# Optimization experiments

Hardware: AMD Instinct MI355X
Metric: run time of the kernel (lower is better)

## Reference

```python
import jax, jax.numpy as jnp
import numpy as np

DN = ('NCDHW', 'OIDHW', 'NCDHW')

def conv3(x, w):
    # 3x3x3 VALID stencil conv: [1,1,D+2,H+2,W+2] -> [1,1,D,H,W]
    return jax.lax.conv_general_dilated(x, w, (1, 1, 1), 'VALID', dimension_numbers=DN)

def conv_res(x, w):
    # 2x2x2 stride-2 restriction
    return jax.lax.conv_general_dilated(x, w, (2, 2, 2), 'VALID', dimension_numbers=DN)

def prol(x):
    for ax in (2, 3, 4):
        x = jnp.repeat(x, 2, axis=ax)
    return x

def with_halo(x, factor=1.0):
    # apply_BC_* + halo_exchange on one device: edge-replicate a 1-cell halo,
    # optionally scaled by `factor` (apply_BC_u uses -1.0 -> no-slip wall).
    p = jnp.pad(x, ((0, 0), (0, 0), (1, 1), (1, 1), (1, 1)), mode='edge')
    if factor != 1.0:
        interior = jnp.pad(jnp.ones_like(x), ((0, 0), (0, 0), (1, 1), (1, 1), (1, 1)))
        p = p * (interior + factor * (1.0 - interior))
    return p

def pad0(x):
    # apply_BC_cw: zero halo for the multigrid correction
    return jnp.pad(x, ((0, 0), (0, 0), (1, 1), (1, 1), (1, 1)))


def setup_inputs() -> dict:
    key = jax.random.key(0)
    ks = jax.random.split(key, 12)
    D = 128
    shp = (1, 1, D, D, D)
    f32 = jnp.float32
    values_u = jax.random.normal(ks[0], shp, f32)
    values_v = jax.random.normal(ks[1], shp, f32)
    values_w = jax.random.normal(ks[2], shp, f32)
    values_p = jax.random.normal(ks[3], shp, f32)
    sigma = jax.random.uniform(ks[4], shp, f32)
    kshape = (1, 1, 3, 3, 3)
    w_xadv = 0.1 * jax.random.normal(ks[5], kshape, f32)
    w_yadv = 0.1 * jax.random.normal(ks[6], kshape, f32)
    w_zadv = 0.1 * jax.random.normal(ks[7], kshape, f32)
    w_diff = 0.1 * jax.random.normal(ks[8], kshape, f32)
    wA = 0.1 * jax.random.normal(ks[9], kshape, f32)
    wA = wA.at[0, 0, 1, 1, 1].add(-6.0)  # Laplacian-like diagonal so Jacobi division is stable
    w_res = 0.1 * jax.random.normal(ks[10], (1, 1, 2, 2, 2), f32)
    dt = 0.05 * jnp.ones((1,), f32)
    return dict(values_u=values_u, values_v=values_v, values_w=values_w,
                values_p=values_p, sigma=sigma, w_xadv=w_xadv, w_yadv=w_yadv,
                w_zadv=w_zadv, w_diff=w_diff, wA=wA, w_res=w_res, dt=dt,
                iteration=2, nlevel=9)


def reference(values_u, values_v, values_w, values_p, sigma, w_xadv, w_yadv,
              w_zadv, w_diff, wA, w_res, dt, iteration, nlevel):
    diag = wA[0, 0, 1, 1, 1]
    xadv = lambda t: conv3(t, w_xadv)
    yadv = lambda t: conv3(t, w_yadv)
    zadv = lambda t: conv3(t, w_zadv)
    diff = lambda t: conv3(t, w_diff)
    A = lambda t: conv3(t, wA)

    def solid(a, b, c):
        d = 1.0 + dt * sigma
        return a / d, b / d, c / d

    def PG(uu, vv, ww, u, v, w):
        # k_u/k_v/k_w are ones; k_uu/k_vv/k_ww are their BC+halo versions (also ones)
        k_h = with_halo(jnp.ones_like(u))
        k_u = 0.5 * (diff(uu) + diff(uu * k_h) - u * diff(k_h))
        k_v = 0.5 * (diff(vv) + diff(vv * k_h) - v * diff(k_h))
        k_w = 0.5 * (diff(ww) + diff(ww * k_h) - w * diff(k_h))
        return k_u, k_v, k_w

    def f_cycle_mg(uu, vv, wwh, p, pp):
        b = -(xadv(uu) + yadv(vv) + zadv(wwh)) / dt
        w_mg = jnp.zeros((1, 1, 1, 1, 1), p.dtype)
        r = b
        for _ in range(iteration):
            w_mg = jnp.zeros((1, 1, 1, 1, 1), p.dtype)
            r = A(pp) - b
            r_s = [r]
            for _i in range(1, nlevel - 1):
                r = conv_res(r, w_res)
                r_s.append(r)
            for i in reversed(range(1, nlevel - 1)):
                ww_ = pad0(w_mg)
                w_mg = w_mg - A(ww_) / diag + r_s[i] / diag
                w_mg = prol(w_mg)
            p = p - w_mg
            p = p - A(pp) / diag + b / diag
            pp = with_halo(p)
        return p, w_mg, r, pp

    u, v, w = solid(values_u, values_v, values_w)
    uu = with_halo(u, -1.0)
    vv = with_halo(v)
    wwh = with_halo(w)
    pp = with_halo(values_p)

    k_u, k_v, k_w = PG(uu, vv, wwh, u, v, w)
    b_u = u + 0.5 * (0.001 * k_u * dt - u * xadv(uu) * dt - v * yadv(uu) * dt - w * zadv(uu) * dt) - xadv(pp) * dt
    b_v = v + 0.5 * (0.001 * k_v * dt - u * xadv(vv) * dt - v * yadv(vv) * dt - w * zadv(vv) * dt) - yadv(pp) * dt
    b_w = w + 0.5 * (0.001 * k_w * dt - u * xadv(wwh) * dt - v * yadv(wwh) * dt - w * zadv(wwh) * dt) - zadv(pp) * dt
    b_u, b_v, b_w = solid(b_u, b_v, b_w)
    b_uu = with_halo(b_u, -1.0)
    b_vv = with_halo(b_v)
    b_ww = with_halo(b_w)

    k_u, k_v, k_w = PG(b_uu, b_vv, b_ww, b_u, b_v, b_w)
    u = u + 0.001 * k_u * dt - b_u * xadv(b_uu) * dt - b_v * yadv(b_uu) * dt - b_w * zadv(b_uu) * dt - xadv(pp) * dt
    v = v + 0.001 * k_v * dt - b_u * xadv(b_vv) * dt - b_v * yadv(b_vv) * dt - b_w * zadv(b_vv) * dt - yadv(pp) * dt
    w = w + 0.001 * k_w * dt - b_u * xadv(b_ww) * dt - b_v * yadv(b_ww) * dt - b_w * zadv(b_ww) * dt - zadv(pp) * dt
    u, v, w = solid(u, v, w)

    uu = with_halo(u, -1.0)
    vv = with_halo(v)
    wwh = with_halo(w)
    p, w_mg, r, pp = f_cycle_mg(uu, vv, wwh, values_p, pp)

    u = u - xadv(pp) * dt
    v = v - yadv(pp) * dt
    w = w - zadv(pp) * dt
    u, v, w = solid(u, v, w)
    return (u, v, w, p, w_mg, r)
```

## Files before the change

### kernel.cpp

```cpp
#include <hip/hip_runtime.h>
#include <stdint.h>


#define NN 128
#define NF (NN*NN*NN)

#define YB 8
#define ZSEG 4
#define RPF 10
#define RW 128
#define FPL (RPF*RW)
#define PL3 (3*FPL)


__device__ __forceinline__ void stage_gld(
    float* __restrict__ slab, int slot, int zp, int y0,
    const float* __restrict__ su, const float* __restrict__ sv,
    const float* __restrict__ sw, int wave, int lane) {
  int gz = min(max(zp, 0), NN-1);
  int halfsel = lane >> 5;
  int xoff = (lane & 31) << 2;
  int cidx = 0;
#pragma unroll
  for (int f = 0; f < 3; ++f) {
    const float* fp = (f == 0) ? su : ((f == 1) ? sv : sw);
#pragma unroll
    for (int q = 0; q < 5; ++q, ++cidx) {
      if ((cidx & 3) != wave) continue;
      int r = 2*q + halfsel;
      int gy = min(max(y0 - 1 + r, 0), NN-1);
      const float* gp = fp + ((size_t)(gz*NN + gy) << 7) + xoff;
      float* lp = slab + (size_t)slot*PL3 + f*FPL + 2*q*RW;
      __builtin_amdgcn_global_load_lds(
          (const __attribute__((address_space(1))) uint32_t*)gp,
          (__attribute__((address_space(3))) uint32_t*)lp, 16, 0, 0);
    }
  }
}


__device__ __forceinline__ void prep9(int z, int y, int rb[9], bool rn[9]) {
  int zi[3] = {z > 0 ? z-1 : 0, z, z < NN-1 ? z+1 : NN-1};
  int yi[3] = {y > 0 ? y-1 : 0, y, y < NN-1 ? y+1 : NN-1};
  bool zo[3] = {z == 0, false, z == NN-1};
  bool yo[3] = {y == 0, false, y == NN-1};
#pragma unroll
  for (int a = 0; a < 3; ++a)
#pragma unroll
    for (int b = 0; b < 3; ++b) {
      rb[a*3+b] = (zi[a]*NN + yi[b])*NN;
      rn[a*3+b] = zo[a] | yo[b];
    }
}

template<bool NEG>
__device__ __forceinline__ void sten4(
    const float* __restrict__ f, const int rb[9], const bool rn[9],
    bool lo, bool hi, int x0,
    const float* __restrict__ w0p, const float* __restrict__ w1p,
    const float* __restrict__ w2p, const float* __restrict__ w3p,
    float acc[4][4], float4* center) {
  const float* const Ws[4] = {w0p, w1p, w2p, w3p};
#pragma unroll
  for (int r = 0; r < 9; ++r) {
    int base = rb[r] + x0;
    float4 c = *(const float4*)(f + base);
    float m1 = f[base - (lo ? 0 : 1)];
    float p4 = f[base + (hi ? 3 : 4)];
    if (NEG) {
      float sr = rn[r] ? -1.f : 1.f;
      m1 *= (rn[r] | lo) ? -1.f : 1.f;
      p4 *= (rn[r] | hi) ? -1.f : 1.f;
      c.x *= sr; c.y *= sr; c.z *= sr; c.w *= sr;
    }
    if (r == 4 && center) *center = c;
    float t[6] = {m1, c.x, c.y, c.z, c.w, p4};
#pragma unroll
    for (int s = 0; s < 4; ++s) {
      const float* W = Ws[s];
      float a0 = W[r*3+0], a1 = W[r*3+1], a2 = W[r*3+2];
#pragma unroll
      for (int k = 0; k < 4; ++k)
        acc[s][k] = fmaf(a0, t[k], fmaf(a1, t[k+1], fmaf(a2, t[k+2], acc[s][k])));
    }
  }
}

__device__ __forceinline__ void sten_p3(
    const float* __restrict__ f, const int rb[9],
    bool lo, bool hi, int x0,
    const float* __restrict__ w0p, const float* __restrict__ w1p,
    const float* __restrict__ w2p, float acc[3][4]) {
  const float* const Ws[3] = {w0p, w1p, w2p};
#pragma unroll
  for (int r = 0; r < 9; ++r) {
    int base = rb[r] + x0;
    float4 c = *(const float4*)(f + base);
    float m1 = f[base - (lo ? 0 : 1)];
    float p4 = f[base + (hi ? 3 : 4)];
    float t[6] = {m1, c.x, c.y, c.z, c.w, p4};
#pragma unroll
    for (int s = 0; s < 3; ++s) {
      const float* W = Ws[s];
      float a0 = W[r*3+0], a1 = W[r*3+1], a2 = W[r*3+2];
#pragma unroll
      for (int k = 0; k < 4; ++k)
        acc[s][k] = fmaf(a0, t[k], fmaf(a1, t[k+1], fmaf(a2, t[k+2], acc[s][k])));
    }
  }
}


__global__ void __launch_bounds__(256) k_prep(
    float* __restrict__ uo, float* __restrict__ vo, float* __restrict__ wo,
    float* __restrict__ gqu, float* __restrict__ gqv, float* __restrict__ gqw,
    float* __restrict__ ap0,
    const float* __restrict__ vu, const float* __restrict__ vv, const float* __restrict__ vw,
    const float* __restrict__ pf, const float* __restrict__ sg,
    const float* __restrict__ wx, const float* __restrict__ wy,
    const float* __restrict__ wz, const float* __restrict__ wA,
    const float* __restrict__ dtp) {
  int x0 = threadIdx.x * 4;
  int y  = blockIdx.x * 8 + threadIdx.y;
  int z  = blockIdx.y;
  bool lo = (x0 == 0), hi = (x0 == NN-4);
  int rb[9]; bool rn[9];
  prep9(z, y, rb, rn);
  float dt = dtp[0];
  int i4 = ((z*NN + y)*NN + x0) >> 2;

  float4 u4 = ((const float4*)vu)[i4];
  float4 v4 = ((const float4*)vv)[i4];
  float4 w4 = ((const float4*)vw)[i4];
  float4 s4 = ((const float4*)sg)[i4];

  float aP[4][4] = {};
  sten4<false>(pf, rb, rn, lo, hi, x0, wx, wy, wz, wA, aP, (float4*)nullptr);

  float uv[4] = {u4.x, u4.y, u4.z, u4.w};
  float vv_[4] = {v4.x, v4.y, v4.z, v4.w};
  float wv[4] = {w4.x, w4.y, w4.z, w4.w};
  float sv[4] = {s4.x, s4.y, s4.z, s4.w};
  float ou[4], ov[4], ow[4], gu[4], gv[4], gw[4];
#pragma unroll
  for (int k = 0; k < 4; ++k) {
    float rd = 1.0f / (1.0f + dt*sv[k]);
    ou[k] = uv[k]*rd; ov[k] = vv_[k]*rd; ow[k] = wv[k]*rd;
    gu[k] = ou[k] - aP[0][k]*dt;
    gv[k] = ov[k] - aP[1][k]*dt;
    gw[k] = ow[k] - aP[2][k]*dt;
  }
  ((float4*)uo)[i4]  = make_float4(ou[0], ou[1], ou[2], ou[3]);
  ((float4*)vo)[i4]  = make_float4(ov[0], ov[1], ov[2], ov[3]);
  ((float4*)wo)[i4]  = make_float4(ow[0], ow[1], ow[2], ow[3]);
  ((float4*)gqu)[i4] = make_float4(gu[0], gu[1], gu[2], gu[3]);
  ((float4*)gqv)[i4] = make_float4(gv[0], gv[1], gv[2], gv[3]);
  ((float4*)gqw)[i4] = make_float4(gw[0], gw[1], gw[2], gw[3]);
  ((float4*)ap0)[i4] = make_float4(aP[3][0], aP[3][1], aP[3][2], aP[3][3]);
}

template<bool NEG>
__device__ __forceinline__ void consume_field(
    const float* __restrict__ slab, int sm, int sc, int sp, int f,
    int yy, int x0, bool lo, bool hi,
    const bool zon[3], const bool yon[3],
    const float* __restrict__ wx, const float* __restrict__ wy,
    const float* __restrict__ wz, const float* __restrict__ wd,
    float acc[4][4], float cen[4]) {
  const float* const Ws[4] = {wx, wy, wz, wd};
  const int slots[3] = {sm, sc, sp};
#pragma unroll
  for (int dz = 0; dz < 3; ++dz) {
    const float* fb = slab + (size_t)slots[dz]*PL3 + f*FPL;
#pragma unroll
    for (int dy = 0; dy < 3; ++dy) {
      const float* row = fb + (yy+dy)*RW;
      float4 c = *(const float4*)(row + x0);
      float m1 = lo ? c.x : row[x0-1];
      float p4 = hi ? c.w : row[x0+4];
      if (NEG) {
        bool rno = zon[dz] | yon[dy];
        float sr = rno ? -1.f : 1.f;
        m1 *= (rno | lo) ? -1.f : 1.f;
        p4 *= (rno | hi) ? -1.f : 1.f;
        c.x *= sr; c.y *= sr; c.z *= sr; c.w *= sr;
      }
      if (dz == 1 && dy == 1) {
        cen[0] = c.x; cen[1] = c.y; cen[2] = c.z; cen[3] = c.w;
      }
      float t[6] = {m1, c.x, c.y, c.z, c.w, p4};
#pragma unroll
      for (int s = 0; s < 4; ++s) {
        const float* W = Ws[s];
        float a0 = W[(dz*3+dy)*3+0], a1 = W[(dz*3+dy)*3+1], a2 = W[(dz*3+dy)*3+2];
#pragma unroll
        for (int k = 0; k < 4; ++k)
          acc[s][k] = fmaf(a0, t[k], fmaf(a1, t[k+1], fmaf(a2, t[k+2], acc[s][k])));
      }
    }
  }
}

__global__ void __launch_bounds__(256) k_mom3_gld(
    float* __restrict__ du, float* __restrict__ dv, float* __restrict__ dw,
    const float* __restrict__ su, const float* __restrict__ sv, const float* __restrict__ sw,
    const float* __restrict__ gqu, const float* __restrict__ gqv, const float* __restrict__ gqw,
    const float* __restrict__ sg,
    const float* __restrict__ wx, const float* __restrict__ wy,
    const float* __restrict__ wz, const float* __restrict__ wd,
    const float* __restrict__ dtp, float scale) {
  __shared__ float slab[4*PL3];
  int tid  = threadIdx.y*32 + threadIdx.x;
  int wave = tid >> 6;
  int lane = tid & 63;
  int x0 = threadIdx.x*4, yy = threadIdx.y;
  int y0 = blockIdx.x * YB;
  int z0 = blockIdx.y * ZSEG;
  int y  = y0 + yy;
  bool lo = (x0 == 0), hi = (x0 == NN-4);
  float dt = dtp[0];

  float sw27 = 0.f;
#pragma unroll
  for (int j = 0; j < 27; ++j) sw27 += wd[j];

  bool yon[3];
  yon[0] = (y == 0); yon[1] = false; yon[2] = (y == NN-1);

  stage_gld(slab, 3, z0-1, y0, su, sv, sw, wave, lane);
  stage_gld(slab, 0, z0,   y0, su, sv, sw, wave, lane);

#pragma unroll
  for (int j = 0; j < ZSEG; ++j) {
    stage_gld(slab, (j+1)&3, z0+j+1, y0, su, sv, sw, wave, lane);
    __syncthreads();
    int z = z0 + j;
    bool zon[3];
    zon[0] = (z == 0); zon[1] = false; zon[2] = (z == NN-1);
    const int sm = (j+3)&3, sc = j&3, sp = (j+1)&3;

    float aU[4][4] = {}, aV[4][4] = {}, aW[4][4] = {};
    float cu4[4], cv4[4], cw4[4];
    consume_field<true >(slab, sm, sc, sp, 0, yy, x0, lo, hi, zon, yon,
                         wx, wy, wz, wd, aU, cu4);
    consume_field<false>(slab, sm, sc, sp, 1, yy, x0, lo, hi, zon, yon,
                         wx, wy, wz, wd, aV, cv4);
    consume_field<false>(slab, sm, sc, sp, 2, yy, x0, lo, hi, zon, yon,
                         wx, wy, wz, wd, aW, cw4);

    int i4 = ((z*NN + y)*NN + x0) >> 2;
    float4 gu4 = ((const float4*)gqu)[i4];
    float4 gv4 = ((const float4*)gqv)[i4];
    float4 gw4 = ((const float4*)gqw)[i4];
    float4 sg4 = ((const float4*)sg)[i4];
    float guv[4] = {gu4.x, gu4.y, gu4.z, gu4.w};
    float gvv[4] = {gv4.x, gv4.y, gv4.z, gv4.w};
    float gwv[4] = {gw4.x, gw4.y, gw4.z, gw4.w};
    float sgv[4] = {sg4.x, sg4.y, sg4.z, sg4.w};
    float ou[4], ov[4], ow[4];
#pragma unroll
    for (int k = 0; k < 4; ++k) {
      float cu = cu4[k], cv = cv4[k], cw = cw4[k];
      float ku = aU[3][k] - 0.5f*sw27*cu;
      float kv = aV[3][k] - 0.5f*sw27*cv;
      float kw = aW[3][k] - 0.5f*sw27*cw;
      float ru = guv[k] + scale*dt*(0.001f*ku - cu*aU[0][k] - cv*aU[1][k] - cw*aU[2][k]);
      float rv = gvv[k] + scale*dt*(0.001f*kv - cu*aV[0][k] - cv*aV[1][k] - cw*aV[2][k]);
      float rw = gwv[k] + scale*dt*(0.001f*kw - cu*aW[0][k] - cv*aW[1][k] - cw*aW[2][k]);
      float rd = 1.0f / (1.0f + dt*sgv[k]);
      ou[k] = ru*rd; ov[k] = rv*rd; ow[k] = rw*rd;
    }
    ((float4*)du)[i4] = make_float4(ou[0], ou[1], ou[2], ou[3]);
    ((float4*)dv)[i4] = make_float4(ov[0], ov[1], ov[2], ov[3]);
    ((float4*)dw)[i4] = make_float4(ow[0], ow[1], ow[2], ow[3]);
  }
}

__global__ void __launch_bounds__(256) k_bdiv_gld(
    float* __restrict__ bb, float* __restrict__ rfine,
    const float* __restrict__ su, const float* __restrict__ sv, const float* __restrict__ sw,
    const float* __restrict__ ap0,
    const float* __restrict__ wx, const float* __restrict__ wy, const float* __restrict__ wz,
    const float* __restrict__ dtp) {
  __shared__ float slab[4*PL3];
  int tid  = threadIdx.y*32 + threadIdx.x;
  int wave = tid >> 6;
  int lane = tid & 63;
  int x0 = threadIdx.x*4, yy = threadIdx.y;
  int y0 = blockIdx.x * YB;
  int z0 = blockIdx.y * ZSEG;
  int y  = y0 + yy;
  bool lo = (x0 == 0), hi = (x0 == NN-4);
  float rdt = 1.0f / dtp[0];

  bool yon[3];
  yon[0] = (y == 0); yon[1] = false; yon[2] = (y == NN-1);

  stage_gld(slab, 3, z0-1, y0, su, sv, sw, wave, lane);
  stage_gld(slab, 0, z0,   y0, su, sv, sw, wave, lane);

#pragma unroll
  for (int j = 0; j < ZSEG; ++j) {
    stage_gld(slab, (j+1)&3, z0+j+1, y0, su, sv, sw, wave, lane);
    __syncthreads();
    int z = z0 + j;
    bool zon[3];
    zon[0] = (z == 0); zon[1] = false; zon[2] = (z == NN-1);
    const int sm = (j+3)&3, sc = j&3, sp = (j+1)&3;
    const int slots[3] = {sm, sc, sp};
    const float* const Ws[3] = {wx, wy, wz};

    float sacc[4] = {};
#pragma unroll
    for (int f = 0; f < 3; ++f) {
      const float* W = Ws[f];
#pragma unroll
      for (int dz = 0; dz < 3; ++dz) {
        const float* fb = slab + (size_t)slots[dz]*PL3 + f*FPL;
#pragma unroll
        for (int dy = 0; dy < 3; ++dy) {
          const float* row = fb + (yy+dy)*RW;
          float4 c = *(const float4*)(row + x0);
          float m1 = lo ? c.x : row[x0-1];
          float p4 = hi ? c.w : row[x0+4];
          if (f == 0) {
            bool rno = zon[dz] | yon[dy];
            float sr = rno ? -1.f : 1.f;
            m1 *= (rno | lo) ? -1.f : 1.f;
            p4 *= (rno | hi) ? -1.f : 1.f;
            c.x *= sr; c.y *= sr; c.z *= sr; c.w *= sr;
          }
          float t[6] = {m1, c.x, c.y, c.z, c.w, p4};
          float a0 = W[(dz*3+dy)*3+0], a1 = W[(dz*3+dy)*3+1], a2 = W[(dz*3+dy)*3+2];
#pragma unroll
          for (int k = 0; k < 4; ++k)
            sacc[k] = fmaf(a0, t[k], fmaf(a1, t[k+1], fmaf(a2, t[k+2], sacc[k])));
        }
      }
    }

    int i4 = ((z*NN + y)*NN + x0) >> 2;
    float4 a4 = ((const float4*)ap0)[i4];
    float av[4] = {a4.x, a4.y, a4.z, a4.w};
    float bv[4], rv[4];
#pragma unroll
    for (int k = 0; k < 4; ++k) {
      bv[k] = -sacc[k]*rdt;
      rv[k] = av[k] - bv[k];
    }
    ((float4*)bb)[i4]    = make_float4(bv[0], bv[1], bv[2], bv[3]);
    ((float4*)rfine)[i4] = make_float4(rv[0], rv[1], rv[2], rv[3]);
  }
}


__device__ __forceinline__ void row4g(const float* __restrict__ f, int base,
                                      bool lo, bool hi, float t[4]) {
  float2 c = *(const float2*)(f + base);
  t[0] = f[base - (lo ? 0 : 1)];
  t[1] = c.x; t[2] = c.y;
  t[3] = f[base + (hi ? 1 : 2)];
}

__device__ __forceinline__ void prep16(int Z, int Y, int rb[16], bool rn[16]) {
  int z0 = 2*Z, y0 = 2*Y;
  int zi[4] = {z0 > 0 ? z0-1 : 0, z0, z0+1, z0+2 < NN ? z0+2 : NN-1};
  int yi[4] = {y0 > 0 ? y0-1 : 0, y0, y0+1, y0+2 < NN ? y0+2 : NN-1};
  bool zo[4] = {Z == 0, false, false, Z == 63};
  bool yo[4] = {Y == 0, false, false, Y == 63};
#pragma unroll
  for (int a = 0; a < 4; ++a)
#pragma unroll
    for (int b = 0; b < 4; ++b) {
      rb[a*4+b] = (zi[a]*NN + yi[b])*NN;
      rn[a*4+b] = zo[a] | yo[b];
    }
}

template<bool NEG>
__device__ __forceinline__ void cc_acc(
    const float* __restrict__ f, const float* __restrict__ W,
    const int rb[16], const bool rn[16], bool lo, bool hi, int x0,
    float out8[8]) {
#pragma unroll
  for (int zp = 0; zp < 4; ++zp) {
    float t[4][4];
#pragma unroll
    for (int yp = 0; yp < 4; ++yp) {
      row4g(f, rb[zp*4+yp] + x0, lo, hi, t[yp]);
      if (NEG) {
        bool rno = rn[zp*4+yp];
        float sr = rno ? -1.f : 1.f;
        t[yp][1] *= sr; t[yp][2] *= sr;
        t[yp][0] *= (rno | lo) ? -1.f : 1.f;
        t[yp][3] *= (rno | hi) ? -1.f : 1.f;
      }
    }
#pragma unroll
    for (int dz = 0; dz < 2; ++dz) {
      int a = zp - dz;
      if (a < 0 || a > 2) continue;
#pragma unroll
      for (int oy = 0; oy < 2; ++oy)
#pragma unroll
        for (int b = 0; b < 3; ++b) {
          const float* tr = t[oy + b];
          float w0 = W[(a*3+b)*3+0], w1 = W[(a*3+b)*3+1], w2 = W[(a*3+b)*3+2];
#pragma unroll
          for (int dx = 0; dx < 2; ++dx)
            out8[(dz*2+oy)*2+dx] =
              fmaf(w0, tr[dx], fmaf(w1, tr[dx+1], fmaf(w2, tr[dx+2], out8[(dz*2+oy)*2+dx])));
        }
    }
  }
}

__global__ void __launch_bounds__(256) k_resres1(
    float* __restrict__ rfine, float* __restrict__ rc1,
    const float* __restrict__ pf, const float* __restrict__ bb,
    const float* __restrict__ wA, const float* __restrict__ wr) {
  int i = blockIdx.x*256 + threadIdx.x;
  if (i >= 64*64*64) return;
  int X = i & 63, Y = (i >> 6) & 63, Z = i >> 12;
  bool lo = (X == 0), hi = (X == 63);
  int x0 = 2*X;
  int rb[16]; bool rn[16];
  prep16(Z, Y, rb, rn);
  float a8[8] = {};
  cc_acc<false>(pf, wA, rb, rn, lo, hi, x0, a8);
  float rsum = 0.f;
#pragma unroll
  for (int f = 0; f < 8; ++f) {
    int dz = f >> 2, dy = (f >> 1) & 1, dx = f & 1;
    int idx = ((2*Z+dz)*NN + (2*Y+dy))*NN + x0 + dx;
    float rcell = a8[f] - bb[idx];
    rfine[idx] = rcell;
    rsum = fmaf(wr[(dz*2+dy)*2+dx], rcell, rsum);
  }
  rc1[i] = rsum;
}

__global__ void __launch_bounds__(256) k_restrict(
    float* __restrict__ dst, const float* __restrict__ src,
    const float* __restrict__ wr, int no) {
  int i = blockIdx.x*256 + threadIdx.x;
  int n3 = no*no*no;
  if (i >= n3) return;
  int x = i % no; int t = i / no; int y = t % no; int z = t / no;
  int ni = 2*no;
  float s = 0.f;
#pragma unroll
  for (int a = 0; a < 2; ++a)
#pragma unroll
    for (int b = 0; b < 2; ++b)
#pragma unroll
      for (int c = 0; c < 2; ++c)
        s = fmaf(wr[(a*2+b)*2+c], src[((2*z+a)*ni + (2*y+b))*ni + (2*x+c)], s);
  dst[i] = s;
}

__device__ __forceinline__ float azb_prol(const float* __restrict__ wh, int hs, int s,
    int z, int y, int x, const float* __restrict__ wA) {
  float acc = 0.f;
#pragma unroll
  for (int a = 0; a < 3; ++a) { int zz = z + a - 1; if ((unsigned)zz >= (unsigned)s) continue;
#pragma unroll
    for (int b = 0; b < 3; ++b) { int yy = y + b - 1; if ((unsigned)yy >= (unsigned)s) continue;
#pragma unroll
      for (int c = 0; c < 3; ++c) { int xx = x + c - 1; if ((unsigned)xx >= (unsigned)s) continue;
        acc = fmaf(wA[(a*3+b)*3+c], wh[((zz>>1)*hs + (yy>>1))*hs + (xx>>1)], acc);
      } } }
  return acc;
}

__global__ void __launch_bounds__(512) k_mg_small(
    float* __restrict__ w16, float* __restrict__ r_o,
    const float* __restrict__ rc2,
    const float* __restrict__ wA, const float* __restrict__ wr) {
  __shared__ float r16[4096];
  __shared__ float r8[512];
  __shared__ float r4[64];
  __shared__ float r2[8];
  __shared__ float wa[512];
  __shared__ float wb[64];
  __shared__ float scal[2];
  int tid = threadIdx.x;
  float diag = wA[13];
  float wrl[8];
#pragma unroll
  for (int j = 0; j < 8; ++j) wrl[j] = wr[j];

  for (int j = tid; j < 4096; j += 512) {
    int x = j & 15, y = (j >> 4) & 15, z = j >> 8;
    float s = 0.f;
#pragma unroll
    for (int a = 0; a < 2; ++a)
#pragma unroll
      for (int b = 0; b < 2; ++b)
#pragma unroll
        for (int c = 0; c < 2; ++c)
          s = fmaf(wrl[(a*2+b)*2+c], rc2[((2*z+a)*32 + (2*y+b))*32 + (2*x+c)], s);
    r16[j] = s;
  }
  __syncthreads();
  {
    int j = tid;
    int x = j & 7, y = (j >> 3) & 7, z = j >> 6;
    float s = 0.f;
#pragma unroll
    for (int a = 0; a < 2; ++a)
#pragma unroll
      for (int b = 0; b < 2; ++b)
#pragma unroll
        for (int c = 0; c < 2; ++c)
          s = fmaf(wrl[(a*2+b)*2+c], r16[((2*z+a)*16 + (2*y+b))*16 + (2*x+c)], s);
    r8[j] = s;
  }
  __syncthreads();
  if (tid < 64) {
    int x = tid & 3, y = (tid >> 2) & 3, z = tid >> 4;
    float s = 0.f;
#pragma unroll
    for (int a = 0; a < 2; ++a)
#pragma unroll
      for (int b = 0; b < 2; ++b)
#pragma unroll
        for (int c = 0; c < 2; ++c)
          s = fmaf(wrl[(a*2+b)*2+c], r8[((2*z+a)*8 + (2*y+b))*8 + (2*x+c)], s);
    r4[tid] = s;
  }
  __syncthreads();
  if (tid < 8) {
    int x = tid & 1, y = (tid >> 1) & 1, z = tid >> 2;
    float s = 0.f;
#pragma unroll
    for (int a = 0; a < 2; ++a)
#pragma unroll
      for (int b = 0; b < 2; ++b)
#pragma unroll
        for (int c = 0; c < 2; ++c)
          s = fmaf(wrl[(a*2+b)*2+c], r4[((2*z+a)*4 + (2*y+b))*4 + (2*x+c)], s);
    r2[tid] = s;
  }
  __syncthreads();
  if (tid == 0) {
    float s = 0.f;
#pragma unroll
    for (int j = 0; j < 8; ++j) s = fmaf(wrl[j], r2[j], s);
    scal[0] = s;
    r_o[0] = s;
    scal[1] = s / diag;
  }
  __syncthreads();
  if (tid < 8) {
    int x = tid & 1, y = (tid >> 1) & 1, z = tid >> 2;
    float wp = scal[1];
    float az = azb_prol(&scal[1], 1, 2, z, y, x, wA);
    wa[tid] = wp - az/diag + r2[tid]/diag;
  }
  __syncthreads();
  if (tid < 64) {
    int x = tid & 3, y = (tid >> 2) & 3, z = tid >> 4;
    float wp = wa[((z>>1)*2 + (y>>1))*2 + (x>>1)];
    float az = azb_prol(wa, 2, 4, z, y, x, wA);
    wb[tid] = wp - az/diag + r4[tid]/diag;
  }
  __syncthreads();
  {
    int j = tid;
    int x = j & 7, y = (j >> 3) & 7, z = j >> 6;
    float wp = wb[((z>>1)*4 + (y>>1))*4 + (x>>1)];
    float az = azb_prol(wb, 4, 8, z, y, x, wA);
    wa[j] = wp - az/diag + r8[j]/diag;
  }
  __syncthreads();
  for (int j = tid; j < 4096; j += 512) {
    int x = j & 15, y = (j >> 4) & 15, z = j >> 8;
    float wp = wa[((z>>1)*8 + (y>>1))*8 + (x>>1)];
    float az = azb_prol(wa, 8, 16, z, y, x, wA);
    w16[j] = wp - az/diag + r16[j]/diag;
  }
}

__global__ void __launch_bounds__(256) k_coarse_step(
    float* __restrict__ wout, const float* __restrict__ wh,
    const float* __restrict__ rl, const float* __restrict__ wA, int s) {
  int i = blockIdx.x*256 + threadIdx.x;
  int n3 = s*s*s;
  if (i >= n3) return;
  int x = i % s; int t = i / s; int y = t % s; int z = t / s;
  int hs = s >> 1;
  float diag = wA[13];
  float wp = wh[((z>>1)*hs + (y>>1))*hs + (x>>1)];
  float az = azb_prol(wh, hs, s, z, y, x, wA);
  wout[i] = wp - az/diag + rl[i]/diag;
}

__global__ void __launch_bounds__(256) k_pupd4(
    float* __restrict__ pdst, float* __restrict__ wmgo,
    const float* __restrict__ psrc, const float* __restrict__ rfine,
    const float* __restrict__ w64, const float* __restrict__ wA, int writeWmg) {
  int i4 = blockIdx.x*256 + threadIdx.x;
  if (i4 >= NF/4) return;
  int i = i4*4;
  int x = i & (NN-1); int t = i >> 7; int y = t & (NN-1); int z = t >> 7;
  float rdiag = 1.0f / wA[13];
  float2 w2 = *(const float2*)(w64 + ((size_t)(z>>1)*64 + (y>>1))*64 + (x>>1));
  float4 ps = ((const float4*)psrc)[i4];
  float4 rf = ((const float4*)rfine)[i4];
  float4 o = make_float4(ps.x - w2.x - rf.x*rdiag,
                         ps.y - w2.x - rf.y*rdiag,
                         ps.z - w2.y - rf.z*rdiag,
                         ps.w - w2.y - rf.w*rdiag);
  ((float4*)pdst)[i4] = o;
  if (writeWmg) ((float4*)wmgo)[i4] = make_float4(w2.x, w2.x, w2.y, w2.y);
}

__global__ void __launch_bounds__(256) k_proj3(
    float* __restrict__ u, float* __restrict__ v, float* __restrict__ w,
    const float* __restrict__ pf, const float* __restrict__ sg,
    const float* __restrict__ wx, const float* __restrict__ wy,
    const float* __restrict__ wz, const float* __restrict__ dtp) {
  int x0 = threadIdx.x * 4;
  int y  = blockIdx.x * 8 + threadIdx.y;
  int z  = blockIdx.y;
  bool lo = (x0 == 0), hi = (x0 == NN-4);
  int rb[9]; bool rn[9];
  prep9(z, y, rb, rn);
  float aP[3][4] = {};
  sten_p3(pf, rb, lo, hi, x0, wx, wy, wz, aP);
  float dt = dtp[0];
  int i4 = ((z*NN + y)*NN + x0) >> 2;
  float4 u4 = ((const float4*)u)[i4];
  float4 v4 = ((const float4*)v)[i4];
  float4 w4 = ((const float4*)w)[i4];
  float4 sg4 = ((const float4*)sg)[i4];
  float ua[4] = {u4.x, u4.y, u4.z, u4.w};
  float va[4] = {v4.x, v4.y, v4.z, v4.w};
  float wa[4] = {w4.x, w4.y, w4.z, w4.w};
  float sa[4] = {sg4.x, sg4.y, sg4.z, sg4.w};
  float ou[4], ov[4], ow[4];
#pragma unroll
  for (int k = 0; k < 4; ++k) {
    float rd = 1.0f / (1.0f + dt*sa[k]);
    ou[k] = (ua[k] - aP[0][k]*dt)*rd;
    ov[k] = (va[k] - aP[1][k]*dt)*rd;
    ow[k] = (wa[k] - aP[2][k]*dt)*rd;
  }
  ((float4*)u)[i4] = make_float4(ou[0], ou[1], ou[2], ou[3]);
  ((float4*)v)[i4] = make_float4(ov[0], ov[1], ov[2], ov[3]);
  ((float4*)w)[i4] = make_float4(ow[0], ow[1], ow[2], ow[3]);
}


extern "C" void kernel_launch(void* const* d_in, const int* in_sizes, int n_in,
                              void* d_out, int out_size, void* d_ws, size_t ws_size,
                              hipStream_t stream) {
  const float* values_u = (const float*)d_in[0];
  const float* values_v = (const float*)d_in[1];
  const float* values_w = (const float*)d_in[2];
  const float* values_p = (const float*)d_in[3];
  const float* sigma    = (const float*)d_in[4];
  const float* wx       = (const float*)d_in[5];
  const float* wy       = (const float*)d_in[6];
  const float* wz       = (const float*)d_in[7];
  const float* wd       = (const float*)d_in[8];
  const float* wA       = (const float*)d_in[9];
  const float* wr       = (const float*)d_in[10];
  const float* dtp      = (const float*)d_in[11];

  float* out   = (float*)d_out;
  float* u_o   = out;
  float* v_o   = out + (size_t)NF;
  float* w_o   = out + (size_t)2*NF;
  float* p_o   = out + (size_t)3*NF;
  float* wmg_o = out + (size_t)4*NF;
  float* r_o   = out + (size_t)5*NF;

  float* ws    = (float*)d_ws;
  float* f0    = ws;
  float* f1    = f0 + (size_t)NF;
  float* f2    = f1 + (size_t)NF;
  float* bws   = f2 + (size_t)NF;
  float* rfine = bws + (size_t)NF;
  float* pbuf  = rfine + (size_t)NF;
  float* gqu   = pbuf + (size_t)NF;
  float* gqv   = gqu + (size_t)NF;
  float* gqw   = gqv + (size_t)NF;
  float* ap0   = gqw + (size_t)NF;
  float* rc1   = ap0 + (size_t)NF;
  float* rc2   = rc1 + 262144;
  float* w16   = rc2 + 32768;
  float* w32   = w16 + 4096;
  float* w64   = w32 + 32768;

  const int TB = 256;
  dim3 blkS(32, 8, 1);
  dim3 grdS(16, 128, 1);
  dim3 blkG(32, 8, 1);
  dim3 grdG(16, 32, 1);

  k_prep<<<grdS, blkS, 0, stream>>>(u_o, v_o, w_o, gqu, gqv, gqw, ap0,
                                    values_u, values_v, values_w, values_p, sigma,
                                    wx, wy, wz, wA, dtp);
  k_mom3_gld<<<grdG, blkG, 0, stream>>>(f0, f1, f2, u_o, v_o, w_o, gqu, gqv, gqw,
                                        sigma, wx, wy, wz, wd, dtp, 0.5f);
  k_mom3_gld<<<grdG, blkG, 0, stream>>>(u_o, v_o, w_o, f0, f1, f2, gqu, gqv, gqw,
                                        sigma, wx, wy, wz, wd, dtp, 1.0f);

  k_bdiv_gld<<<grdG, blkG, 0, stream>>>(bws, rfine, u_o, v_o, w_o, ap0,
                                        wx, wy, wz, dtp);
  k_restrict<<<1024, TB, 0, stream>>>(rc1, rfine, wr, 64);
  k_restrict<<<128, TB, 0, stream>>>(rc2, rc1, wr, 32);
  k_mg_small<<<1, 512, 0, stream>>>(w16, r_o, rc2, wA, wr);
  k_coarse_step<<<128, TB, 0, stream>>>(w32, w16, rc2, wA, 32);
  k_coarse_step<<<1024, TB, 0, stream>>>(w64, w32, rc1, wA, 64);
  k_pupd4<<<NF/4/TB, TB, 0, stream>>>(pbuf, wmg_o, values_p, rfine, w64, wA, 0);

  k_resres1<<<1024, TB, 0, stream>>>(rfine, rc1, pbuf, bws, wA, wr);
  k_restrict<<<128, TB, 0, stream>>>(rc2, rc1, wr, 32);
  k_mg_small<<<1, 512, 0, stream>>>(w16, r_o, rc2, wA, wr);
  k_coarse_step<<<128, TB, 0, stream>>>(w32, w16, rc2, wA, 32);
  k_coarse_step<<<1024, TB, 0, stream>>>(w64, w32, rc1, wA, 64);
  k_pupd4<<<NF/4/TB, TB, 0, stream>>>(p_o, wmg_o, pbuf, rfine, w64, wA, 1);

  k_proj3<<<grdS, blkS, 0, stream>>>(u_o, v_o, w_o, p_o, sigma, wx, wy, wz, dtp);
}
```

Measured before the change: 222.0 us.

## Deepen LDS prefetch to two planes and replace fused residual-restrict kernel

Measured after the change: 225.1 us. Within noise of the previous version (+1.4%).

```diff
diff --git a/kernel.cpp b/kernel.cpp
--- a/kernel.cpp
+++ b/kernel.cpp
@@ -12,29 +12,57 @@
 #define FPL (RPF*RW)
 #define PL3 (3*FPL)
 
-
-__device__ __forceinline__ void stage_gld(
+__device__ __forceinline__ void wait_vmcnt4() {
+  asm volatile("s_waitcnt vmcnt(4)" ::: "memory");
+}
+__device__ __forceinline__ void wait_vmcnt2() {
+  asm volatile("s_waitcnt vmcnt(2)" ::: "memory");
+}
+__device__ __forceinline__ void memfence() {
+  asm volatile("" ::: "memory");
+}
+
+
+__device__ __forceinline__ void stage16(
     float* __restrict__ slab, int slot, int zp, int y0,
     const float* __restrict__ su, const float* __restrict__ sv,
     const float* __restrict__ sw, int wave, int lane) {
   int gz = min(max(zp, 0), NN-1);
   int halfsel = lane >> 5;
   int xoff = (lane & 31) << 2;
-  int cidx = 0;
-#pragma unroll
-  for (int f = 0; f < 3; ++f) {
+#pragma unroll
+  for (int cidx = 0; cidx < 16; ++cidx) {
+    if ((cidx & 3) != wave) continue;
+    int f = cidx < 5 ? 0 : (cidx < 10 ? 1 : 2);
+    int q = cidx < 5 ? cidx : (cidx < 10 ? cidx-5 : (cidx < 15 ? cidx-10 : 4));
     const float* fp = (f == 0) ? su : ((f == 1) ? sv : sw);
-#pragma unroll
-    for (int q = 0; q < 5; ++q, ++cidx) {
-      if ((cidx & 3) != wave) continue;
-      int r = 2*q + halfsel;
-      int gy = min(max(y0 - 1 + r, 0), NN-1);
-      const float* gp = fp + ((size_t)(gz*NN + gy) << 7) + xoff;
-      float* lp = slab + (size_t)slot*PL3 + f*FPL + 2*q*RW;
-      __builtin_amdgcn_global_load_lds(
-          (const __attribute__((address_space(1))) uint32_t*)gp,
-          (__attribute__((address_space(3))) uint32_t*)lp, 16, 0, 0);
-    }
+    int r = 2*q + halfsel;
+    int gy = min(max(y0 - 1 + r, 0), NN-1);
+    const float* gp = fp + ((size_t)(gz*NN + gy) << 7) + xoff;
+    float* lp = slab + (size_t)slot*PL3 + f*FPL + 2*q*RW;
+    __builtin_amdgcn_global_load_lds(
+        (const __attribute__((address_space(1))) uint32_t*)gp,
+        (__attribute__((address_space(3))) uint32_t*)lp, 16, 0, 0);
+  }
+}
+
+__device__ __forceinline__ void stage8(
+    float* __restrict__ slab, int slot, int zp, int y0,
+    const float* __restrict__ fp, int wave, int lane) {
+  int gz = min(max(zp, 0), NN-1);
+  int halfsel = lane >> 5;
+  int xoff = (lane & 31) << 2;
+#pragma unroll
+  for (int cidx = 0; cidx < 8; ++cidx) {
+    if ((cidx & 3) != wave) continue;
+    int q = cidx < 5 ? cidx : cidx - 5;
+    int r = 2*q + halfsel;
+    int gy = min(max(y0 - 1 + r, 0), NN-1);
+    const float* gp = fp + ((size_t)(gz*NN + gy) << 7) + xoff;
+    float* lp = slab + (size_t)slot*FPL + 2*q*RW;
+    __builtin_amdgcn_global_load_lds(
+        (const __attribute__((address_space(1))) uint32_t*)gp,
+        (__attribute__((address_space(3))) uint32_t*)lp, 16, 0, 0);
   }
 }
 
@@ -227,13 +255,17 @@
   bool yon[3];
   yon[0] = (y == 0); yon[1] = false; yon[2] = (y == NN-1);
 
-  stage_gld(slab, 3, z0-1, y0, su, sv, sw, wave, lane);
-  stage_gld(slab, 0, z0,   y0, su, sv, sw, wave, lane);
+  stage16(slab, 3, z0-1, y0, su, sv, sw, wave, lane);
+  stage16(slab, 0, z0,   y0, su, sv, sw, wave, lane);
+  stage16(slab, 1, z0+1, y0, su, sv, sw, wave, lane);
 
 #pragma unroll
   for (int j = 0; j < ZSEG; ++j) {
-    stage_gld(slab, (j+1)&3, z0+j+1, y0, su, sv, sw, wave, lane);
-    __syncthreads();
+    stage16(slab, (j+2)&3, z0+j+2, y0, su, sv, sw, wave, lane);
+    wait_vmcnt4();
+    __builtin_amdgcn_s_barrier();
+    memfence();
+
     int z = z0 + j;
     bool zon[3];
     zon[0] = (z == 0); zon[1] = false; zon[2] = (z == NN-1);
@@ -273,6 +305,9 @@
     ((float4*)du)[i4] = make_float4(ou[0], ou[1], ou[2], ou[3]);
     ((float4*)dv)[i4] = make_float4(ov[0], ov[1], ov[2], ov[3]);
     ((float4*)dw)[i4] = make_float4(ow[0], ow[1], ow[2], ow[3]);
+
+    memfence();
+    __builtin_amdgcn_s_barrier();
   }
 }
 
@@ -296,13 +331,17 @@
   bool yon[3];
   yon[0] = (y == 0); yon[1] = false; yon[2] = (y == NN-1);
 
-  stage_gld(slab, 3, z0-1, y0, su, sv, sw, wave, lane);
-  stage_gld(slab, 0, z0,   y0, su, sv, sw, wave, lane);
+  stage16(slab, 3, z0-1, y0, su, sv, sw, wave, lane);
+  stage16(slab, 0, z0,   y0, su, sv, sw, wave, lane);
+  stage16(slab, 1, z0+1, y0, su, sv, sw, wave, lane);
 
 #pragma unroll
   for (int j = 0; j < ZSEG; ++j) {
-    stage_gld(slab, (j+1)&3, z0+j+1, y0, su, sv, sw, wave, lane);
-    __syncthreads();
+    stage16(slab, (j+2)&3, z0+j+2, y0, su, sv, sw, wave, lane);
+    wait_vmcnt4();
+    __builtin_amdgcn_s_barrier();
+    memfence();
+
     int z = z0 + j;
     bool zon[3];
     zon[0] = (z == 0); zon[1] = false; zon[2] = (z == NN-1);
@@ -350,95 +389,68 @@
     }
     ((float4*)bb)[i4]    = make_float4(bv[0], bv[1], bv[2], bv[3]);
     ((float4*)rfine)[i4] = make_float4(rv[0], rv[1], rv[2], rv[3]);
-  }
-}
-
-
-__device__ __forceinline__ void row4g(const float* __restrict__ f, int base,
-                                      bool lo, bool hi, float t[4]) {
-  float2 c = *(const float2*)(f + base);
-  t[0] = f[base - (lo ? 0 : 1)];
-  t[1] = c.x; t[2] = c.y;
-  t[3] = f[base + (hi ? 1 : 2)];
-}
-
-__device__ __forceinline__ void prep16(int Z, int Y, int rb[16], bool rn[16]) {
-  int z0 = 2*Z, y0 = 2*Y;
-  int zi[4] = {z0 > 0 ? z0-1 : 0, z0, z0+1, z0+2 < NN ? z0+2 : NN-1};
-  int yi[4] = {y0 > 0 ? y0-1 : 0, y0, y0+1, y0+2 < NN ? y0+2 : NN-1};
-  bool zo[4] = {Z == 0, false, false, Z == 63};
-  bool yo[4] = {Y == 0, false, false, Y == 63};
-#pragma unroll
-  for (int a = 0; a < 4; ++a)
-#pragma unroll
-    for (int b = 0; b < 4; ++b) {
-      rb[a*4+b] = (zi[a]*NN + yi[b])*NN;
-      rn[a*4+b] = zo[a] | yo[b];
-    }
-}
-
-template<bool NEG>
-__device__ __forceinline__ void cc_acc(
-    const float* __restrict__ f, const float* __restrict__ W,
-    const int rb[16], const bool rn[16], bool lo, bool hi, int x0,
-    float out8[8]) {
-#pragma unroll
-  for (int zp = 0; zp < 4; ++zp) {
-    float t[4][4];
-#pragma unroll
-    for (int yp = 0; yp < 4; ++yp) {
-      row4g(f, rb[zp*4+yp] + x0, lo, hi, t[yp]);
-      if (NEG) {
-        bool rno = rn[zp*4+yp];
-        float sr = rno ? -1.f : 1.f;
-        t[yp][1] *= sr; t[yp][2] *= sr;
-        t[yp][0] *= (rno | lo) ? -1.f : 1.f;
-        t[yp][3] *= (rno | hi) ? -1.f : 1.f;
+
+    memfence();
+    __builtin_amdgcn_s_barrier();
+  }
+}
+
+__global__ void __launch_bounds__(256) k_res_gld(
+    float* __restrict__ rfine,
+    const float* __restrict__ pf, const float* __restrict__ bb,
+    const float* __restrict__ wA) {
+  __shared__ float slab[4*FPL];
+  int tid  = threadIdx.y*32 + threadIdx.x;
+  int wave = tid >> 6;
+  int lane = tid & 63;
+  int x0 = threadIdx.x*4, yy = threadIdx.y;
+  int y0 = blockIdx.x * YB;
+  int z0 = blockIdx.y * ZSEG;
+  int y  = y0 + yy;
+  bool lo = (x0 == 0), hi = (x0 == NN-4);
+
+  stage8(slab, 3, z0-1, y0, pf, wave, lane);
+  stage8(slab, 0, z0,   y0, pf, wave, lane);
+  stage8(slab, 1, z0+1, y0, pf, wave, lane);
+
+#pragma unroll
+  for (int j = 0; j < ZSEG; ++j) {
+    stage8(slab, (j+2)&3, z0+j+2, y0, pf, wave, lane);
+    wait_vmcnt2();
+    __builtin_amdgcn_s_barrier();
+    memfence();
+
+    int z = z0 + j;
+    const int sm = (j+3)&3, sc = j&3, sp = (j+1)&3;
+    const int slots[3] = {sm, sc, sp};
+
+    float sacc[4] = {};
+#pragma unroll
+    for (int dz = 0; dz < 3; ++dz) {
+      const float* fb = slab + (size_t)slots[dz]*FPL;
+#pragma unroll
+      for (int dy = 0; dy < 3; ++dy) {
+        const float* row = fb + (yy+dy)*RW;
+        float4 c = *(const float4*)(row + x0);
+        float m1 = lo ? c.x : row[x0-1];
+        float p4 = hi ? c.w : row[x0+4];
+        float t[6] = {m1, c.x, c.y, c.z, c.w, p4};
+        float a0 = wA[(dz*3+dy)*3+0], a1 = wA[(dz*3+dy)*3+1], a2 = wA[(dz*3+dy)*3+2];
+#pragma unroll
+        for (int k = 0; k < 4; ++k)
+          sacc[k] = fmaf(a0, t[k], fmaf(a1, t[k+1], fmaf(a2, t[k+2], sacc[k])));
       }
     }
-#pragma unroll
-    for (int dz = 0; dz < 2; ++dz) {
-      int a = zp - dz;
-      if (a < 0 || a > 2) continue;
-#pragma unroll
-      for (int oy = 0; oy < 2; ++oy)
-#pragma unroll
-        for (int b = 0; b < 3; ++b) {
-          const float* tr = t[oy + b];
-          float w0 = W[(a*3+b)*3+0], w1 = W[(a*3+b)*3+1], w2 = W[(a*3+b)*3+2];
-#pragma unroll
-          for (int dx = 0; dx < 2; ++dx)
-            out8[(dz*2+oy)*2+dx] =
-              fmaf(w0, tr[dx], fmaf(w1, tr[dx+1], fmaf(w2, tr[dx+2], out8[(dz*2+oy)*2+dx])));
-        }
-    }
-  }
-}
-
-__global__ void __launch_bounds__(256) k_resres1(
-    float* __restrict__ rfine, float* __restrict__ rc1,
-    const float* __restrict__ pf, const float* __restrict__ bb,
-    const float* __restrict__ wA, const float* __restrict__ wr) {
-  int i = blockIdx.x*256 + threadIdx.x;
-  if (i >= 64*64*64) return;
-  int X = i & 63, Y = (i >> 6) & 63, Z = i >> 12;
-  bool lo = (X == 0), hi = (X == 63);
-  int x0 = 2*X;
-  int rb[16]; bool rn[16];
-  prep16(Z, Y, rb, rn);
-  float a8[8] = {};
-  cc_acc<false>(pf, wA, rb, rn, lo, hi, x0, a8);
-  float rsum = 0.f;
-#pragma unroll
-  for (int f = 0; f < 8; ++f) {
-    int dz = f >> 2, dy = (f >> 1) & 1, dx = f & 1;
-    int idx = ((2*Z+dz)*NN + (2*Y+dy))*NN + x0 + dx;
-    float rcell = a8[f] - bb[idx];
-    rfine[idx] = rcell;
-    rsum = fmaf(wr[(dz*2+dy)*2+dx], rcell, rsum);
-  }
-  rc1[i] = rsum;
-}
+
+    int i4 = ((z*NN + y)*NN + x0) >> 2;
+    float4 b4 = ((const float4*)bb)[i4];
+    ((float4*)rfine)[i4] = make_float4(sacc[0]-b4.x, sacc[1]-b4.y,
+                                       sacc[2]-b4.z, sacc[3]-b4.w);
+    memfence();
+    __builtin_amdgcn_s_barrier();
+  }
+}
+
 
 __global__ void __launch_bounds__(256) k_restrict(
     float* __restrict__ dst, const float* __restrict__ src,
@@ -717,7 +729,8 @@
   k_coarse_step<<<1024, TB, 0, stream>>>(w64, w32, rc1, wA, 64);
   k_pupd4<<<NF/4/TB, TB, 0, stream>>>(pbuf, wmg_o, values_p, rfine, w64, wA, 0);
 
-  k_resres1<<<1024, TB, 0, stream>>>(rfine, rc1, pbuf, bws, wA, wr);
+  k_res_gld<<<grdG, blkG, 0, stream>>>(rfine, pbuf, bws, wA);
+  k_restrict<<<1024, TB, 0, stream>>>(rc1, rfine, wr, 64);
   k_restrict<<<128, TB, 0, stream>>>(rc2, rc1, wr, 32);
   k_mg_small<<<1, 512, 0, stream>>>(w16, r_o, rc2, wA, wr);
   k_coarse_step<<<128, TB, 0, stream>>>(w32, w16, rc2, wA, 32);
```
